# Performance work log

Hardware: AMD Instinct MI355X
Metric: run time of the kernel (lower is better)

## Reference

```python
import jax, jax.numpy as jnp
import numpy as np


def setup_inputs() -> dict:
    key = jax.random.key(0)
    k1, k2, k3, k4, k5 = jax.random.split(key, 5)
    bs, ns, seq_len = 32, 512, 1024
    n_heads, d_r, d_model = 8, 64, 256
    return {
        "x": jax.random.normal(k1, (bs, ns, seq_len), dtype=jnp.float32),
        "routers": jax.random.normal(k2, (n_heads, d_r, d_model), dtype=jnp.float32),
        "w_kv_weight": jax.random.normal(k3, (n_heads * d_model, seq_len), dtype=jnp.float32) * 0.02,
        "proj_weight": jax.random.normal(k4, (seq_len, n_heads * d_model), dtype=jnp.float32) * 0.02,
        "proj_bias": jax.random.normal(k5, (seq_len,), dtype=jnp.float32) * 0.02,
    }


def reference(x, routers, w_kv_weight, proj_weight, proj_bias):
    # x: (bs, ns, seq_len); routers: (H, d_r, d_model)
    bs, ns, _ = x.shape
    H, d_r, d_model = routers.shape
    qk_scale = 1.0 / jnp.sqrt(jnp.asarray(d_model, x.dtype))
    # shared K=V projection: (bs, ns, H*d_model) -> (bs, H, ns, d_model)
    kv = (x @ w_kv_weight.T).reshape(bs, ns, H, d_model).transpose(0, 2, 1, 3)
    # low-rank learned queries attend over the ns axis: (bs, H, d_r, ns)
    attn_score = jnp.einsum('hrd,bhnd->bhrn', routers, kv) * qk_scale
    attn_weight = jax.nn.softmax(attn_score, axis=-1)
    # dropout is identity in eval/reference mode
    out = jnp.einsum('bhrn,bhnd->bhrd', attn_weight, kv)  # (bs, H, d_r, d_model)
    out = out.transpose(0, 2, 1, 3).reshape(bs, d_r, H * d_model)
    out = out @ proj_weight.T + proj_bias  # (bs, d_r, seq_len)
    return out, attn_weight
```

## Files before the change

### kernel.cpp

```cpp
#include <hip/hip_runtime.h>
#include <hip/hip_bf16.h>


typedef __attribute__((ext_vector_type(8))) short short8;
typedef __attribute__((ext_vector_type(4))) short short4v;
typedef __attribute__((ext_vector_type(4))) float f32x4;
typedef __attribute__((ext_vector_type(4))) unsigned int uint4v;
typedef __attribute__((ext_vector_type(4))) unsigned short ushort4v;

__device__ inline unsigned short f2bf(float f) {
  unsigned int u = __float_as_uint(f);
  u += 0x7FFFu + ((u >> 16) & 1u);
  return (unsigned short)(u >> 16);
}

__device__ __forceinline__ void async_copy16(unsigned short* lds, const unsigned short* g) {
  __builtin_amdgcn_global_load_lds(
      (const __attribute__((address_space(1))) unsigned int*)g,
      (__attribute__((address_space(3))) unsigned int*)lds,
      16, 0, 0);
}

__global__ __launch_bounds__(256) void cast_all(
    const float* __restrict__ x, const float* __restrict__ wkv, const float* __restrict__ projw,
    unsigned short* __restrict__ xb, unsigned short* __restrict__ wkv_b,
    unsigned short* __restrict__ projw_b) {
  int i = blockIdx.x * 256 + threadIdx.x;
  const float* src; unsigned short* dst; int off;
  if (i < 524288)        { src = wkv;   dst = wkv_b;   off = i; }
  else if (i < 1048576)  { src = projw; dst = projw_b; off = i - 524288; }
  else                   { src = x;     dst = xb;      off = i - 1048576; }
  float4 v = ((const float4*)src)[off];
  ushort4v w; w.x = f2bf(v.x); w.y = f2bf(v.y); w.z = f2bf(v.z); w.w = f2bf(v.w);
  ((ushort4v*)dst)[off] = w;
}

__global__ __launch_bounds__(512, 1) void gemm1_8phase(
    const unsigned short* __restrict__ A, const unsigned short* __restrict__ B,
    unsigned short* __restrict__ C, int lda, int ldb, int ldc, int K, int nWGn)
{
  __shared__ __align__(16) unsigned short sA[2][2][8192];
  __shared__ __align__(16) unsigned short sB[2][2][8192];

  const int tid = threadIdx.x;
  const int cpx = gridDim.x >> 3;
  const int swz = (blockIdx.x & 7) * cpx + (blockIdx.x >> 3);
  const int bn = swz % nWGn, bm = swz / nWGn;

  const int wave = tid >> 6, lane = tid & 63;
  const int wm = wave >> 2, wn = wave & 3;
  const int lr = lane & 15, ls = lane >> 4;
  const int lsw8 = (ls ^ ((lr >> 1) & 3)) * 8;

  const int r0 = tid >> 2;
  const int sl0 = (tid & 3) ^ ((tid >> 3) & 3);
  const unsigned short* gA = A + (long long)(bm * 256 + r0) * lda + sl0 * 8;
  const unsigned short* gB = B + (long long)(bn * 256 + r0) * ldb + sl0 * 8;
  const long long lda128 = (long long)128 * lda, ldb128 = (long long)128 * ldb;

#define STA(b_, k_, t_) { const unsigned short* g_ = gA + (t_) * 64 + (k_) * 32; \
    async_copy16(&sA[b_][k_][tid * 8], g_); \
    async_copy16(&sA[b_][k_][4096 + tid * 8], g_ + lda128); }
#define STB(b_, k_, t_) { const unsigned short* g_ = gB + (t_) * 64 + (k_) * 32; \
    async_copy16(&sB[b_][k_][tid * 8], g_); \
    async_copy16(&sB[b_][k_][4096 + tid * 8], g_ + ldb128); }

  f32x4 acc[8][4];
  #pragma unroll
  for (int mi = 0; mi < 8; ++mi)
    #pragma unroll
    for (int ni = 0; ni < 4; ++ni)
      acc[mi][ni] = f32x4{0.f, 0.f, 0.f, 0.f};

  const int KT = K >> 6;
  STB(0, 0, 0) STA(0, 0, 0) STB(0, 1, 0) STA(0, 1, 0)
  if (KT > 1) {
    STB(1, 0, 1) STA(1, 0, 1) STB(1, 1, 1)
    asm volatile("s_waitcnt vmcnt(6)" ::: "memory");
  } else {
    asm volatile("s_waitcnt vmcnt(0)" ::: "memory");
  }
  __builtin_amdgcn_s_barrier();
  __builtin_amdgcn_sched_barrier(0);

  for (int t = 0; t < KT; ++t) {
    const int b = t & 1, nb = b ^ 1;
    const bool hasT1 = (t + 1) < KT, hasT2 = (t + 2) < KT;
    short8 af[4], bf[4];

    #pragma unroll
    for (int mi = 0; mi < 4; ++mi)
      af[mi] = *(const short8*)&sA[b][0][(wm * 128 + mi * 16 + lr) * 32 + lsw8];
    #pragma unroll
    for (int ni = 0; ni < 4; ++ni)
      bf[ni] = *(const short8*)&sB[b][0][(wn * 64 + ni * 16 + lr) * 32 + lsw8];
    if (hasT1) { STA(nb, 1, t + 1) }
    __builtin_amdgcn_s_setprio(1);
    #pragma unroll
    for (int mi = 0; mi < 4; ++mi)
      #pragma unroll
      for (int ni = 0; ni < 4; ++ni)
        acc[mi][ni] = __builtin_amdgcn_mfma_f32_16x16x32_bf16(af[mi], bf[ni], acc[mi][ni], 0, 0, 0);
    __builtin_amdgcn_s_setprio(0);
    __builtin_amdgcn_s_barrier();

    #pragma unroll
    for (int mi = 0; mi < 4; ++mi)
      af[mi] = *(const short8*)&sA[b][0][(wm * 128 + (4 + mi) * 16 + lr) * 32 + lsw8];
    if (hasT2) { STB(b, 0, t + 2) }
    __builtin_amdgcn_s_setprio(1);
    #pragma unroll
    for (int mi = 0; mi < 4; ++mi)
      #pragma unroll
      for (int ni = 0; ni < 4; ++ni)
        acc[4 + mi][ni] = __builtin_amdgcn_mfma_f32_16x16x32_bf16(af[mi], bf[ni], acc[4 + mi][ni], 0, 0, 0);
    __builtin_amdgcn_s_setprio(0);
    __builtin_amdgcn_s_barrier();

    #pragma unroll
    for (int mi = 0; mi < 4; ++mi)
      af[mi] = *(const short8*)&sA[b][1][(wm * 128 + mi * 16 + lr) * 32 + lsw8];
    #pragma unroll
    for (int ni = 0; ni < 4; ++ni)
      bf[ni] = *(const short8*)&sB[b][1][(wn * 64 + ni * 16 + lr) * 32 + lsw8];
    if (hasT2) { STA(b, 0, t + 2) }
    __builtin_amdgcn_s_setprio(1);
    #pragma unroll
    for (int mi = 0; mi < 4; ++mi)
      #pragma unroll
      for (int ni = 0; ni < 4; ++ni)
        acc[mi][ni] = __builtin_amdgcn_mfma_f32_16x16x32_bf16(af[mi], bf[ni], acc[mi][ni], 0, 0, 0);
    __builtin_amdgcn_s_setprio(0);
    __builtin_amdgcn_s_barrier();

    #pragma unroll
    for (int mi = 0; mi < 4; ++mi)
      af[mi] = *(const short8*)&sA[b][1][(wm * 128 + (4 + mi) * 16 + lr) * 32 + lsw8];
    if (hasT2) { STB(b, 1, t + 2) }
    __builtin_amdgcn_s_setprio(1);
    #pragma unroll
    for (int mi = 0; mi < 4; ++mi)
      #pragma unroll
      for (int ni = 0; ni < 4; ++ni)
        acc[4 + mi][ni] = __builtin_amdgcn_mfma_f32_16x16x32_bf16(af[mi], bf[ni], acc[4 + mi][ni], 0, 0, 0);
    __builtin_amdgcn_s_setprio(0);
    if (t == KT - 2) {
      asm volatile("s_waitcnt vmcnt(0)" ::: "memory");
    } else if (t < KT - 2) {
      asm volatile("s_waitcnt vmcnt(6)" ::: "memory");
    }
    __builtin_amdgcn_s_barrier();
    __builtin_amdgcn_sched_barrier(0);
  }
#undef STA
#undef STB

  #pragma unroll
  for (int mi = 0; mi < 8; ++mi) {
    #pragma unroll
    for (int ni = 0; ni < 4; ++ni) {
      int row = bm * 256 + wm * 128 + mi * 16 + ls * 4;
      int col = bn * 256 + wn * 64 + ni * 16 + lr;
      #pragma unroll
      for (int r = 0; r < 4; ++r)
        C[(long long)(row + r) * ldc + col] = f2bf(acc[mi][ni][r]);
    }
  }
}

__global__ __launch_bounds__(1024, 1) void score_softmax(
    const float* __restrict__ routers,
    const unsigned short* __restrict__ kv,
    float* __restrict__ attnw,
    unsigned short* __restrict__ P)
{
  __shared__ __align__(16) unsigned short lds_a[64 * 72];
  __shared__ __align__(16) unsigned short lds_b[512 * 72];
  __shared__ float redmax[64][4];
  __shared__ float redsum[64][4];

  const int bh = blockIdx.x;
  const int b = bh >> 3, h = bh & 7;
  const int tid = threadIdx.x;
  const int wave = tid >> 6, lane = tid & 63;
  const int wm = wave >> 2, wn = wave & 3;
  const int lr = lane & 15, ls = lane >> 4;
  const int lk = ls * 8;

  const unsigned short* kvb = kv + (long long)b * 512 * 2048 + h * 256;
  const float* Rh = routers + h * 16384;

  f32x4 acc[8];
  #pragma unroll
  for (int ni = 0; ni < 8; ++ni) acc[ni] = f32x4{0.f, 0.f, 0.f, 0.f};

  for (int k0 = 0; k0 < 256; k0 += 64) {
    {
      int r = tid >> 4, kc = (tid & 15) * 4;
      float4 v = *(const float4*)(Rh + r * 256 + k0 + kc);
      ushort4v w; w.x = f2bf(v.x); w.y = f2bf(v.y); w.z = f2bf(v.z); w.w = f2bf(v.w);
      *(ushort4v*)&lds_a[r * 72 + kc] = w;
    }
    #pragma unroll
    for (int i = 0; i < 4; ++i) {
      int c = i * 1024 + tid;
      int r = c >> 3, kc = (c & 7) * 8;
      *(uint4v*)&lds_b[r * 72 + kc] = *(const uint4v*)(kvb + (long long)r * 2048 + k0 + kc);
    }
    __syncthreads();
    #pragma unroll
    for (int kk = 0; kk < 2; ++kk) {
      short8 af = *(const short8*)&lds_a[(wm * 16 + lr) * 72 + kk * 32 + lk];
      #pragma unroll
      for (int ni = 0; ni < 8; ++ni) {
        short8 bf = *(const short8*)&lds_b[(wn * 128 + ni * 16 + lr) * 72 + kk * 32 + lk];
        acc[ni] = __builtin_amdgcn_mfma_f32_16x16x32_bf16(af, bf, acc[ni], 0, 0, 0);
      }
    }
    __syncthreads();
  }

  #pragma unroll
  for (int q = 0; q < 4; ++q) {
    int row = wm * 16 + ls * 4 + q;
    float m = -1e30f;
    #pragma unroll
    for (int ni = 0; ni < 8; ++ni) { acc[ni][q] *= 0.0625f; m = fmaxf(m, acc[ni][q]); }
    #pragma unroll
    for (int d = 1; d < 16; d <<= 1) m = fmaxf(m, __shfl_xor(m, d, 64));
    if (lr == 0) redmax[row][wn] = m;
  }
  __syncthreads();
  #pragma unroll
  for (int q = 0; q < 4; ++q) {
    int row = wm * 16 + ls * 4 + q;
    float M = fmaxf(fmaxf(redmax[row][0], redmax[row][1]), fmaxf(redmax[row][2], redmax[row][3]));
    float s = 0.f;
    #pragma unroll
    for (int ni = 0; ni < 8; ++ni) { float p = __expf(acc[ni][q] - M); acc[ni][q] = p; s += p; }
    #pragma unroll
    for (int d = 1; d < 16; d <<= 1) s += __shfl_xor(s, d, 64);
    if (lr == 0) redsum[row][wn] = s;
  }
  __syncthreads();
  #pragma unroll
  for (int q = 0; q < 4; ++q) {
    int row = wm * 16 + ls * 4 + q;
    float inv = 1.0f / (redsum[row][0] + redsum[row][1] + redsum[row][2] + redsum[row][3]);
    long long base = (long long)bh * 32768 + row * 512 + wn * 128;
    #pragma unroll
    for (int ni = 0; ni < 8; ++ni) {
      float wv = acc[ni][q] * inv;
      attnw[base + ni * 16 + lr] = wv;
      P[base + ni * 16 + lr] = f2bf(wv);
    }
  }
}

template<int BM,int BN,int BK,int WM,int WN,bool TRANS_B,bool A_F32,bool OUT_BF16,bool DO_SCALE,bool DO_BIAS>
__global__ __launch_bounds__(256) void gemm_bt(
    const void* __restrict__ Av, const unsigned short* __restrict__ Bp,
    void* __restrict__ Cv, const float* __restrict__ bias,
    int lda, int ldb, int ldc, int K, int nWGn,
    long long strAo, long long strAi, long long strBo, long long strBi,
    long long strCo, long long strCi, int binner, float scale)
{
  constexpr int PADA = 8;
  constexpr int PADB = TRANS_B ? 4 : 8;
  constexpr int STRA = BK + PADA;
  constexpr int STRB = BK + PADB;
  constexpr int NWN = BN / WN;
  constexpr int MF = WM / 16, NF = WN / 16;
  __shared__ __align__(16) unsigned short lds_a[BM * STRA];
  __shared__ __align__(16) unsigned short lds_b[BN * STRB];

  const int tid = threadIdx.x;
  const int bn = blockIdx.x % nWGn;
  const int bm = blockIdx.x / nWGn;
  const int batch = blockIdx.y;
  const int bo = batch / binner, bi = batch % binner;

  const int wave = tid >> 6, lane = tid & 63;
  const int wm = wave / NWN, wn = wave % NWN;
  const int lr = lane & 15;
  const int lk = (lane >> 4) * 8;

  const long long abase = bo*strAo + bi*strAi + (long long)bm*BM*lda;
  const long long bbase = bo*strBo + bi*strBi;

  f32x4 acc[MF][NF];
  #pragma unroll
  for (int mi = 0; mi < MF; ++mi)
    #pragma unroll
    for (int ni = 0; ni < NF; ++ni)
      acc[mi][ni] = f32x4{0.f, 0.f, 0.f, 0.f};

  for (int k0 = 0; k0 < K; k0 += BK) {
    if constexpr (A_F32) {
      const float* Af = (const float*)Av + abase + k0;
      #pragma unroll
      for (int i = 0; i < BM*BK/1024; ++i) {
        int c = i*256 + tid;
        int r = c / (BK/4);
        int kc = (c % (BK/4)) * 4;
        float4 v = *(const float4*)(Af + (long long)r*lda + kc);
        ushort4v w; w.x=f2bf(v.x); w.y=f2bf(v.y); w.z=f2bf(v.z); w.w=f2bf(v.w);
        *(ushort4v*)&lds_a[r*STRA + kc] = w;
      }
    } else {
      const unsigned short* Ab2 = (const unsigned short*)Av + abase + k0;
      #pragma unroll
      for (int i = 0; i < BM*BK/2048; ++i) {
        int c = i*256 + tid;
        int r = c / (BK/8);
        int kc = (c % (BK/8)) * 8;
        *(uint4v*)&lds_a[r*STRA + kc] = *(const uint4v*)(Ab2 + (long long)r*lda + kc);
      }
    }
    if constexpr (!TRANS_B) {
      const unsigned short* Bb2 = Bp + bbase + (long long)bn*BN*ldb + k0;
      #pragma unroll
      for (int i = 0; i < BN*BK/2048; ++i) {
        int c = i*256 + tid;
        int r = c / (BK/8);
        int kc = (c % (BK/8)) * 8;
        *(uint4v*)&lds_b[r*STRB + kc] = *(const uint4v*)(Bb2 + (long long)r*ldb + kc);
      }
    } else {
      const unsigned short* Bb2 = Bp + bbase + (long long)k0*ldb + (long long)bn*BN;
      #pragma unroll
      for (int i = 0; i < BN*BK/2048; ++i) {
        int c = i*256 + tid;
        int kr = c / (BN/8);
        int nc = (c % (BN/8)) * 8;
        uint4v v = *(const uint4v*)(Bb2 + (long long)kr*ldb + nc);
        const unsigned short* pv = (const unsigned short*)&v;
        #pragma unroll
        for (int j = 0; j < 8; ++j) lds_b[(nc+j)*STRB + kr] = pv[j];
      }
    }
    __syncthreads();

    #pragma unroll
    for (int kk = 0; kk < BK/32; ++kk) {
      short8 af[MF]; short8 bfr[NF];
      #pragma unroll
      for (int mi = 0; mi < MF; ++mi)
        af[mi] = *(const short8*)&lds_a[(wm*WM + mi*16 + lr)*STRA + kk*32 + lk];
      #pragma unroll
      for (int ni = 0; ni < NF; ++ni) {
        if constexpr (TRANS_B) {
          int base = (wn*WN + ni*16 + lr)*STRB + kk*32 + lk;
          short4v lo = *(const short4v*)&lds_b[base];
          short4v hi = *(const short4v*)&lds_b[base + 4];
          short8 t; t[0]=lo[0]; t[1]=lo[1]; t[2]=lo[2]; t[3]=lo[3];
                    t[4]=hi[0]; t[5]=hi[1]; t[6]=hi[2]; t[7]=hi[3];
          bfr[ni] = t;
        } else {
          bfr[ni] = *(const short8*)&lds_b[(wn*WN + ni*16 + lr)*STRB + kk*32 + lk];
        }
      }
      #pragma unroll
      for (int mi = 0; mi < MF; ++mi)
        #pragma unroll
        for (int ni = 0; ni < NF; ++ni)
          acc[mi][ni] = __builtin_amdgcn_mfma_f32_16x16x32_bf16(af[mi], bfr[ni], acc[mi][ni], 0, 0, 0);
    }
    __syncthreads();
  }

  const long long cbase = bo*strCo + bi*strCi;
  const int cr0 = (lane >> 4) * 4;
  #pragma unroll
  for (int mi = 0; mi < MF; ++mi) {
    #pragma unroll
    for (int ni = 0; ni < NF; ++ni) {
      int row = bm*BM + wm*WM + mi*16 + cr0;
      int col = bn*BN + wn*WN + ni*16 + lr;
      float badd = DO_BIAS ? bias[col] : 0.f;
      #pragma unroll
      for (int r = 0; r < 4; ++r) {
        float x = acc[mi][ni][r];
        if constexpr (DO_SCALE) x *= scale;
        x += badd;
        long long addr = cbase + (long long)(row + r)*ldc + col;
        if constexpr (OUT_BF16) ((unsigned short*)Cv)[addr] = f2bf(x);
        else                    ((float*)Cv)[addr] = x;
      }
    }
  }
}

extern "C" void kernel_launch(void* const* d_in, const int* in_sizes, int n_in,
                              void* d_out, int out_size, void* d_ws, size_t ws_size,
                              hipStream_t stream) {
  const float* x       = (const float*)d_in[0];
  const float* routers = (const float*)d_in[1];
  const float* wkv     = (const float*)d_in[2];
  const float* projw   = (const float*)d_in[3];
  const float* pbias   = (const float*)d_in[4];

  char* ws = (char*)d_ws;
  unsigned short* wkv_b   = (unsigned short*)(ws);
  unsigned short* projw_b = (unsigned short*)(ws +  4194304);
  unsigned short* kv_b    = (unsigned short*)(ws +  8388608);
  unsigned short* xb      = (unsigned short*)(ws + 75497472);
  unsigned short* P_b     = (unsigned short*)(ws + 75759616);
  unsigned short* ao_b    = (unsigned short*)(ws + 92536832);

  float* out0  = (float*)d_out;
  float* attnw = out0 + 2097152;

  cast_all<<<20480, 256, 0, stream>>>(x, wkv, projw, xb, wkv_b, projw_b);

  gemm1_8phase<<<512, 512, 0, stream>>>(xb, wkv_b, kv_b, 1024, 1024, 2048, 1024, 8);

  score_softmax<<<256, 1024, 0, stream>>>(routers, kv_b, attnw, P_b);

  gemm_bt<64,128,64,64,32,true,false,true,false,false><<<dim3(2,256), 256, 0, stream>>>(
      P_b, kv_b, ao_b, nullptr, 512, 2048, 2048, 512, 2,
      262144, 32768, 1048576, 256, 131072, 256, 8, 1.0f);

  gemm_bt<64,128,64,64,32,false,false,false,false,true><<<dim3(256,1), 256, 0, stream>>>(
      ao_b, projw_b, out0, pbias, 2048, 2048, 1024, 2048, 8,
      0,0, 0,0, 0,0, 1, 1.0f);
}
```

Measured before the change: 171.0 us.

## Fuse attention-weighted value GEMM into score/softmax kernel via LDS

The P·V product now runs inside the score/softmax kernel. The bf16 attention weights stay in LDS instead of going out to global memory, and each block transposes its KV slice into LDS in four chunks before running MFMA on them. This removes one kernel launch and the global write and re-read of P. The cost is a much larger LDS footprint (about 148 KB), scalar-transposed LDS stores that may cause bank conflicts, and a P·V phase done by a single block per (batch, head) with limited parallelism.

```diff
diff --git a/kernel.cpp b/kernel.cpp
--- a/kernel.cpp
+++ b/kernel.cpp
@@ -168,16 +168,19 @@
   }
 }
 
-__global__ __launch_bounds__(1024, 1) void score_softmax(
+__global__ __launch_bounds__(1024, 1) void score_softmax_pv(
     const float* __restrict__ routers,
     const unsigned short* __restrict__ kv,
     float* __restrict__ attnw,
-    unsigned short* __restrict__ P)
+    unsigned short* __restrict__ ao)
 {
-  __shared__ __align__(16) unsigned short lds_a[64 * 72];
-  __shared__ __align__(16) unsigned short lds_b[512 * 72];
-  __shared__ float redmax[64][4];
-  __shared__ float redsum[64][4];
+  __shared__ __align__(16) char smem[151552];
+  unsigned short* lds_a = (unsigned short*)smem;
+  unsigned short* lds_b = (unsigned short*)(smem + 9216);
+  unsigned short* P_lds = (unsigned short*)(smem + 9216);
+  unsigned short* kvT   = (unsigned short*)(smem + 82944);
+  float* redmax = (float*)(smem + 149504);
+  float* redsum = (float*)(smem + 150528);
 
   const int bh = blockIdx.x;
   const int b = bh >> 3, h = bh & 7;
@@ -228,32 +231,60 @@
     for (int ni = 0; ni < 8; ++ni) { acc[ni][q] *= 0.0625f; m = fmaxf(m, acc[ni][q]); }
     #pragma unroll
     for (int d = 1; d < 16; d <<= 1) m = fmaxf(m, __shfl_xor(m, d, 64));
-    if (lr == 0) redmax[row][wn] = m;
+    if (lr == 0) redmax[row * 4 + wn] = m;
   }
   __syncthreads();
   #pragma unroll
   for (int q = 0; q < 4; ++q) {
     int row = wm * 16 + ls * 4 + q;
-    float M = fmaxf(fmaxf(redmax[row][0], redmax[row][1]), fmaxf(redmax[row][2], redmax[row][3]));
+    float M = fmaxf(fmaxf(redmax[row * 4 + 0], redmax[row * 4 + 1]),
+                    fmaxf(redmax[row * 4 + 2], redmax[row * 4 + 3]));
     float s = 0.f;
     #pragma unroll
     for (int ni = 0; ni < 8; ++ni) { float p = __expf(acc[ni][q] - M); acc[ni][q] = p; s += p; }
     #pragma unroll
     for (int d = 1; d < 16; d <<= 1) s += __shfl_xor(s, d, 64);
-    if (lr == 0) redsum[row][wn] = s;
+    if (lr == 0) redsum[row * 4 + wn] = s;
   }
   __syncthreads();
   #pragma unroll
   for (int q = 0; q < 4; ++q) {
     int row = wm * 16 + ls * 4 + q;
-    float inv = 1.0f / (redsum[row][0] + redsum[row][1] + redsum[row][2] + redsum[row][3]);
+    float inv = 1.0f / (redsum[row * 4 + 0] + redsum[row * 4 + 1] +
+                        redsum[row * 4 + 2] + redsum[row * 4 + 3]);
     long long base = (long long)bh * 32768 + row * 512 + wn * 128;
     #pragma unroll
     for (int ni = 0; ni < 8; ++ni) {
       float wv = acc[ni][q] * inv;
       attnw[base + ni * 16 + lr] = wv;
-      P[base + ni * 16 + lr] = f2bf(wv);
-    }
+      P_lds[row * 520 + wn * 128 + ni * 16 + lr] = f2bf(wv);
+    }
+  }
+
+  for (int dt = 0; dt < 4; ++dt) {
+    #pragma unroll
+    for (int i = 0; i < 4; ++i) {
+      int c = i * 1024 + tid;
+      int n = c & 511, dgrp = c >> 9;
+      uint4v v = *(const uint4v*)&kvb[(long long)n * 2048 + dt * 64 + dgrp * 8];
+      const unsigned short* pv = (const unsigned short*)&v;
+      #pragma unroll
+      for (int j = 0; j < 8; ++j) kvT[(dgrp * 8 + j) * 520 + n] = pv[j];
+    }
+    __syncthreads();
+    f32x4 accp = f32x4{0.f, 0.f, 0.f, 0.f};
+    #pragma unroll
+    for (int kk = 0; kk < 16; ++kk) {
+      short8 af = *(const short8*)&P_lds[(wm * 16 + lr) * 520 + kk * 32 + lk];
+      short8 bf = *(const short8*)&kvT[(wn * 16 + lr) * 520 + kk * 32 + lk];
+      accp = __builtin_amdgcn_mfma_f32_16x16x32_bf16(af, bf, accp, 0, 0, 0);
+    }
+    #pragma unroll
+    for (int q = 0; q < 4; ++q) {
+      int r = wm * 16 + ls * 4 + q;
+      ao[(long long)(b * 64 + r) * 2048 + h * 256 + dt * 64 + wn * 16 + lr] = f2bf(accp[q]);
+    }
+    __syncthreads();
   }
 }
 
@@ -405,7 +436,6 @@
   unsigned short* projw_b = (unsigned short*)(ws +  4194304);
   unsigned short* kv_b    = (unsigned short*)(ws +  8388608);
   unsigned short* xb      = (unsigned short*)(ws + 75497472);
-  unsigned short* P_b     = (unsigned short*)(ws + 75759616);
   unsigned short* ao_b    = (unsigned short*)(ws + 92536832);
 
   float* out0  = (float*)d_out;
@@ -415,11 +445,7 @@
 
   gemm1_8phase<<<512, 512, 0, stream>>>(xb, wkv_b, kv_b, 1024, 1024, 2048, 1024, 8);
 
-  score_softmax<<<256, 1024, 0, stream>>>(routers, kv_b, attnw, P_b);
-
-  gemm_bt<64,128,64,64,32,true,false,true,false,false><<<dim3(2,256), 256, 0, stream>>>(
-      P_b, kv_b, ao_b, nullptr, 512, 2048, 2048, 512, 2,
-      262144, 32768, 1048576, 256, 131072, 256, 8, 1.0f);
+  score_softmax_pv<<<256, 1024, 0, stream>>>(routers, kv_b, attnw, ao_b);
 
   gemm_bt<64,128,64,64,32,false,false,false,false,true><<<dim3(256,1), 256, 0, stream>>>(
       ao_b, projw_b, out0, pbias, 2048, 2048, 1024, 2048, 8,
```

Measured after the change: 163.2 us. 4.6% less time.
